# Kernel optimization log

Measured on AMD Instinct MI355X. Metric: run time of the kernel, lower is better.

## Reference

```python
import jax, jax.numpy as jnp
import numpy as np

B, S, H, L, O = 128, 2048, 128, 2, 2  # batch, seq, hidden(=input), layers, output


def setup_inputs() -> dict:
    key = jax.random.key(0)
    k1, k2, k3, k4, k5 = jax.random.split(key, 5)
    std = 1.0 / np.sqrt(H)
    x_data = jax.random.normal(k1, (B, S, H), dtype=jnp.float32)
    x_length = jax.random.randint(k2, (B,), 0, S, dtype=jnp.int32)
    x_label = jax.random.uniform(k3, (B,), dtype=jnp.float32)
    # torch Linear layout: y = x @ W.T ; init uniform(-1/sqrt(H), 1/sqrt(H))
    Wx2h = jax.random.uniform(k4, (L, 2 * H, H), minval=-std, maxval=std, dtype=jnp.float32)
    Wfc = jax.random.uniform(k5, (L, O, H), minval=-std, maxval=std, dtype=jnp.float32)
    return {"x_data": x_data, "x_length": x_length, "x_label": x_label,
            "Wx2h": Wx2h, "Wfc": Wfc}


def reference(x_data, x_length, x_label, Wx2h, Wfc):
    Bn, Sn, Hn = x_data.shape
    Ln = Wx2h.shape[0]
    # valid-timestep mask: seq index < x_length[i]
    mask = (jnp.arange(Sn)[None, :] < x_length[:, None]).astype(x_data.dtype)  # [B,S]

    def step(carry, inp):
        S1, S2 = carry            # each [L,B,H]
        x_t, m_t = inp            # [B,H], [B]
        h = x_t
        out = None
        S1_new, S2_new = [], []
        for l in range(Ln):
            gate = h @ Wx2h[l].T                    # [B,2H]
            m1, m2 = jnp.split(gate, 2, axis=1)
            s1n = S1[l] + jnp.tanh(m1)
            s2n = S2[l] + jnp.tanh(m2)
            Fu = jax.nn.relu(s1n)
            h = (1.0 - Fu) * s2n + Fu * S2[l]       # hy
            out = jax.nn.softmax(h @ Wfc[l].T, axis=1)  # [B,O]
            S1_new.append(s1n)
            S2_new.append(s2n)
        loss_t = m_t * (x_label - jax.nn.sigmoid(out[:, 1])) ** 2  # [B]
        return (jnp.stack(S1_new), jnp.stack(S2_new)), loss_t

    S0 = jnp.zeros((Ln, Bn, Hn), x_data.dtype)
    xs = (jnp.swapaxes(x_data, 0, 1), mask.T)  # time-major [S,B,H], [S,B]
    _, losses = jax.lax.scan(step, (S0, S0), xs)
    return jnp.sum(losses)
```

## Files before the change

### kernel.cpp

```cpp
#include <hip/hip_runtime.h>

typedef __bf16 bf16;
typedef __bf16 bf16x8 __attribute__((ext_vector_type(8)));
typedef float floatx4 __attribute__((ext_vector_type(4)));

#define BATCH 128
#define SEQ   2048
#define HID   128
#define TWOH  256
#define CH    128
#define NCH   16
#define MTOT  (BATCH * SEQ)

__device__ __forceinline__ float fast_tanh(float x) {
    float e = __builtin_amdgcn_exp2f(2.88539008177793f * x);
    return 1.0f - 2.0f * __builtin_amdgcn_rcpf(e + 1.0f);
}
__device__ __forceinline__ float fast_sigmoid(float x) {
    return __builtin_amdgcn_rcpf(1.0f + __builtin_amdgcn_exp2f(-1.44269504088896f * x));
}

union PK4 { unsigned long long u; bf16 h[4]; };
union PK8 { uint4 u; bf16 h[8]; };

__global__ __launch_bounds__(256) void convert_w_k(const float* __restrict__ W,
                                                   bf16* __restrict__ Wb) {
    int i = blockIdx.x * 256 + threadIdx.x;
    float4 v = ((const float4*)W)[i];
    PK4 pk;
    pk.h[0] = (bf16)v.x; pk.h[1] = (bf16)v.y;
    pk.h[2] = (bf16)v.z; pk.h[3] = (bf16)v.w;
    ((unsigned long long*)Wb)[i] = pk.u;
}

__device__ __forceinline__ void tile_prefix(const float g[4][4], float pref[4][4],
                                            float* stripe_tot, int quad, int l16) {
    float mibase = 0.f;
    #pragma unroll
    for (int mi = 0; mi < 4; ++mi) {
        float s0 = g[mi][0];
        float s1 = s0 + g[mi][1];
        float s2 = s1 + g[mi][2];
        float s3 = s2 + g[mi][3];
        float tot = s3, xq = tot;
        float t = __shfl_up(xq, 16);
        if (quad >= 1) xq += t;
        t = __shfl_up(xq, 32);
        if (quad >= 2) xq += t;
        float excl = mibase + xq - tot;
        pref[mi][0] = excl + s0;
        pref[mi][1] = excl + s1;
        pref[mi][2] = excl + s2;
        pref[mi][3] = excl + s3;
        mibase += __shfl(xq, 48 + l16);
    }
    *stripe_tot = mibase;
}


__global__ __launch_bounds__(512, 4) void l0_k(const float* __restrict__ x,
                                               const bf16* __restrict__ Wb,
                                               uint4* __restrict__ T,
                                               float* __restrict__ Pout) {
    __shared__ bf16 As[128 * 128];
    __shared__ bf16 Bs[128 * 128];
    __shared__ float psum[512];

    const int tid  = threadIdx.x;
    const int lane = tid & 63;
    const int wid  = tid >> 6;
    const int wr   = wid >> 2;
    const int wc   = wid & 3;
    const int quad = lane >> 4;
    const int l16  = lane & 15;
    const long blk = blockIdx.x;
    const long rowBase = blk * 128;

    {
        const float4* A4 = (const float4*)(x + rowBase * HID);
        #pragma unroll
        for (int it = 0; it < 8; ++it) {
            int i  = it * 512 + tid;
            int r  = i >> 5;
            int c4 = i & 31;
            float4 v = A4[i];
            int g = c4 >> 1, hf = c4 & 1;
            PK4 pk;
            pk.h[0] = (bf16)v.x; pk.h[1] = (bf16)v.y;
            pk.h[2] = (bf16)v.z; pk.h[3] = (bf16)v.w;
            *(unsigned long long*)&As[r * 128 + ((g ^ (r & 7)) << 3) + (hf << 2)] = pk.u;
        }
    }

    #pragma unroll
    for (int half = 0; half < 2; ++half) {
        __syncthreads();
        {
            const uint4* W8 = (const uint4*)(Wb + (size_t)half * 128 * HID);
            #pragma unroll
            for (int it = 0; it < 4; ++it) {
                int i = it * 512 + tid;
                int r = i >> 4;
                int g = i & 15;
                uint4 v = W8[i];
                *(uint4*)&Bs[r * 128 + ((g ^ (r & 7)) << 3)] = v;
            }
        }
        __syncthreads();

        floatx4 acc[4][2];
        #pragma unroll
        for (int a = 0; a < 4; ++a)
            #pragma unroll
            for (int b2 = 0; b2 < 2; ++b2) acc[a][b2] = (floatx4){0.f, 0.f, 0.f, 0.f};

        #pragma unroll
        for (int kk = 0; kk < 128; kk += 32) {
            bf16x8 af[4], bfr[2];
            int kg = (kk >> 3) + quad;
            #pragma unroll
            for (int mi = 0; mi < 4; ++mi) {
                int r = wr * 64 + mi * 16 + l16;
                af[mi] = *(const bf16x8*)&As[r * 128 + ((kg ^ (r & 7)) << 3)];
            }
            #pragma unroll
            for (int ni = 0; ni < 2; ++ni) {
                int n = wc * 32 + ni * 16 + l16;
                bfr[ni] = *(const bf16x8*)&Bs[n * 128 + ((kg ^ (n & 7)) << 3)];
            }
            #pragma unroll
            for (int mi = 0; mi < 4; ++mi)
                #pragma unroll
                for (int ni = 0; ni < 2; ++ni)
                    acc[mi][ni] = __builtin_amdgcn_mfma_f32_16x16x32_bf16(
                        af[mi], bfr[ni], acc[mi][ni], 0, 0, 0);
        }

        float g2[2][4][4];
        #pragma unroll
        for (int mi = 0; mi < 4; ++mi)
            #pragma unroll
            for (int ni = 0; ni < 2; ++ni)
                #pragma unroll
                for (int rr = 0; rr < 4; ++rr)
                    g2[ni][mi][rr] = fast_tanh(acc[mi][ni][rr]);

        #pragma unroll
        for (int mi = 0; mi < 4; ++mi) {
            PK8 p;
            #pragma unroll
            for (int rr = 0; rr < 4; ++rr) {
                p.h[rr]     = (bf16)g2[0][mi][rr];
                p.h[4 + rr] = (bf16)g2[1][mi][rr];
            }
            T[((blk * 2 + half) * 4 + mi) * 512 + tid] = p.u;
        }

        #pragma unroll
        for (int ni = 0; ni < 2; ++ni) {
            float cs = 0.f;
            #pragma unroll
            for (int mi = 0; mi < 4; ++mi)
                #pragma unroll
                for (int rr = 0; rr < 4; ++rr) cs += g2[ni][mi][rr];
            cs += __shfl_xor(cs, 16);
            cs += __shfl_xor(cs, 32);
            if (quad == 0)
                psum[wr * 256 + half * 128 + wc * 32 + ni * 16 + l16] = cs;
        }
    }

    __syncthreads();
    if (tid < 256) Pout[(blk << 8) + tid] = psum[tid] + psum[256 + tid];
}

__global__ __launch_bounds__(256) void scan_partials_k(float* __restrict__ P) {
    int ch = threadIdx.x;
    long b = blockIdx.x;
    float v[NCH];
    #pragma unroll
    for (int c = 0; c < NCH; ++c) v[c] = P[((b * NCH + c) << 8) + ch];
    float run = 0.f;
    #pragma unroll
    for (int c = 0; c < NCH; ++c) {
        float t = v[c];
        P[((b * NCH + c) << 8) + ch] = run;
        run += t;
    }
}

__global__ __launch_bounds__(512, 4) void l1_k(const bf16* __restrict__ Wb1,
                                               uint4* __restrict__ T,
                                               const float* __restrict__ P0,
                                               float* __restrict__ Pout) {
    __shared__ bf16 As[128 * 128];
    __shared__ bf16 Bs[128 * 128];
    __shared__ float auxp[128];
    __shared__ float psum[512];

    const int tid  = threadIdx.x;
    const int lane = tid & 63;
    const int wid  = tid >> 6;
    const int wr   = wid >> 2;
    const int wc   = wid & 3;
    const int quad = lane >> 4;
    const int l16  = lane & 15;
    const long blk = blockIdx.x;

    float p1[2][4][4];

    {
        float g2[2][4][4];
        #pragma unroll
        for (int mi = 0; mi < 4; ++mi) {
            PK8 p;
            p.u = T[((blk * 2 + 0) * 4 + mi) * 512 + tid];
            #pragma unroll
            for (int rr = 0; rr < 4; ++rr) {
                g2[0][mi][rr] = (float)p.h[rr];
                g2[1][mi][rr] = (float)p.h[4 + rr];
            }
        }
        float pref[2][4][4], st[2];
        #pragma unroll
        for (int ni = 0; ni < 2; ++ni) {
            tile_prefix(g2[ni], pref[ni], &st[ni], quad, l16);
            if (wr == 0 && quad == 0) auxp[wc * 32 + ni * 16 + l16] = st[ni];
        }
        __syncthreads();
        #pragma unroll
        for (int ni = 0; ni < 2; ++ni) {
            int col = wc * 32 + ni * 16 + l16;
            float off = P0[(blk << 8) + col];
            if (wr) off += auxp[col];
            #pragma unroll
            for (int mi = 0; mi < 4; ++mi)
                #pragma unroll
                for (int rr = 0; rr < 4; ++rr)
                    p1[ni][mi][rr] = pref[ni][mi][rr] + off;
        }
    }
    __syncthreads();

    {
        float g2[2][4][4];
        #pragma unroll
        for (int mi = 0; mi < 4; ++mi) {
            PK8 p;
            p.u = T[((blk * 2 + 1) * 4 + mi) * 512 + tid];
            #pragma unroll
            for (int rr = 0; rr < 4; ++rr) {
                g2[0][mi][rr] = (float)p.h[rr];
                g2[1][mi][rr] = (float)p.h[4 + rr];
            }
        }
        float pref[2][4][4], st[2];
        #pragma unroll
        for (int ni = 0; ni < 2; ++ni) {
            tile_prefix(g2[ni], pref[ni], &st[ni], quad, l16);
            if (wr == 0 && quad == 0) auxp[wc * 32 + ni * 16 + l16] = st[ni];
        }
        __syncthreads();
        #pragma unroll
        for (int ni = 0; ni < 2; ++ni) {
            int col = wc * 32 + ni * 16 + l16;
            int gsw = col >> 3, rem = col & 7;
            float off = P0[(blk << 8) + 128 + col];
            if (wr) off += auxp[col];
            #pragma unroll
            for (int mi = 0; mi < 4; ++mi)
                #pragma unroll
                for (int rr = 0; rr < 4; ++rr) {
                    int row = wr * 64 + mi * 16 + quad * 4 + rr;
                    float h = pref[ni][mi][rr] + off -
                              fmaxf(p1[ni][mi][rr], 0.f) * g2[ni][mi][rr];
                    As[row * 128 + ((gsw ^ (row & 7)) << 3) + rem] = (bf16)h;
                }
        }
    }

    #pragma unroll
    for (int half = 0; half < 2; ++half) {
        __syncthreads();
        {
            const uint4* W8 = (const uint4*)(Wb1 + (size_t)half * 128 * HID);
            #pragma unroll
            for (int it = 0; it < 4; ++it) {
                int i = it * 512 + tid;
                int r = i >> 4;
                int g = i & 15;
                uint4 v = W8[i];
                *(uint4*)&Bs[r * 128 + ((g ^ (r & 7)) << 3)] = v;
            }
        }
        __syncthreads();

        floatx4 acc[4][2];
        #pragma unroll
        for (int a = 0; a < 4; ++a)
            #pragma unroll
            for (int b2 = 0; b2 < 2; ++b2) acc[a][b2] = (floatx4){0.f, 0.f, 0.f, 0.f};

        #pragma unroll
        for (int kk = 0; kk < 128; kk += 32) {
            bf16x8 af[4], bfr[2];
            int kg = (kk >> 3) + quad;
            #pragma unroll
            for (int mi = 0; mi < 4; ++mi) {
                int r = wr * 64 + mi * 16 + l16;
                af[mi] = *(const bf16x8*)&As[r * 128 + ((kg ^ (r & 7)) << 3)];
            }
            #pragma unroll
            for (int ni = 0; ni < 2; ++ni) {
                int n = wc * 32 + ni * 16 + l16;
                bfr[ni] = *(const bf16x8*)&Bs[n * 128 + ((kg ^ (n & 7)) << 3)];
            }
            #pragma unroll
            for (int mi = 0; mi < 4; ++mi)
                #pragma unroll
                for (int ni = 0; ni < 2; ++ni)
                    acc[mi][ni] = __builtin_amdgcn_mfma_f32_16x16x32_bf16(
                        af[mi], bfr[ni], acc[mi][ni], 0, 0, 0);
        }

        float g2[2][4][4];
        #pragma unroll
        for (int mi = 0; mi < 4; ++mi)
            #pragma unroll
            for (int ni = 0; ni < 2; ++ni)
                #pragma unroll
                for (int rr = 0; rr < 4; ++rr)
                    g2[ni][mi][rr] = fast_tanh(acc[mi][ni][rr]);

        #pragma unroll
        for (int mi = 0; mi < 4; ++mi) {
            PK8 p;
            #pragma unroll
            for (int rr = 0; rr < 4; ++rr) {
                p.h[rr]     = (bf16)g2[0][mi][rr];
                p.h[4 + rr] = (bf16)g2[1][mi][rr];
            }
            T[((blk * 2 + half) * 4 + mi) * 512 + tid] = p.u;
        }

        #pragma unroll
        for (int ni = 0; ni < 2; ++ni) {
            float cs = 0.f;
            #pragma unroll
            for (int mi = 0; mi < 4; ++mi)
                #pragma unroll
                for (int rr = 0; rr < 4; ++rr) cs += g2[ni][mi][rr];
            cs += __shfl_xor(cs, 16);
            cs += __shfl_xor(cs, 32);
            if (quad == 0)
                psum[wr * 256 + half * 128 + wc * 32 + ni * 16 + l16] = cs;
        }
    }

    __syncthreads();
    if (tid < 256) Pout[(blk << 8) + tid] = psum[tid] + psum[256 + tid];
}

__global__ __launch_bounds__(512, 4) void loss_k(const uint4* __restrict__ T,
                                                 const float* __restrict__ P1,
                                                 const float* __restrict__ Wfc,
                                                 const int* __restrict__ xlen,
                                                 const float* __restrict__ xlab,
                                                 float* __restrict__ out) {
    __shared__ float auxp[128];
    __shared__ float zbuf[4][128][2];
    __shared__ float red[2];

    const int tid  = threadIdx.x;
    const int lane = tid & 63;
    const int wid  = tid >> 6;
    const int wr   = wid >> 2;
    const int wc   = wid & 3;
    const int quad = lane >> 4;
    const int l16  = lane & 15;
    const long blk = blockIdx.x;

    float p1[2][4][4];

    {
        float g2[2][4][4];
        #pragma unroll
        for (int mi = 0; mi < 4; ++mi) {
            PK8 p;
            p.u = T[((blk * 2 + 0) * 4 + mi) * 512 + tid];
            #pragma unroll
            for (int rr = 0; rr < 4; ++rr) {
                g2[0][mi][rr] = (float)p.h[rr];
                g2[1][mi][rr] = (float)p.h[4 + rr];
            }
        }
        float pref[2][4][4], st[2];
        #pragma unroll
        for (int ni = 0; ni < 2; ++ni) {
            tile_prefix(g2[ni], pref[ni], &st[ni], quad, l16);
            if (wr == 0 && quad == 0) auxp[wc * 32 + ni * 16 + l16] = st[ni];
        }
        __syncthreads();
        #pragma unroll
        for (int ni = 0; ni < 2; ++ni) {
            int col = wc * 32 + ni * 16 + l16;
            float off = P1[(blk << 8) + col];
            if (wr) off += auxp[col];
            #pragma unroll
            for (int mi = 0; mi < 4; ++mi)
                #pragma unroll
                for (int rr = 0; rr < 4; ++rr)
                    p1[ni][mi][rr] = pref[ni][mi][rr] + off;
        }
    }
    __syncthreads();

    {
        float g2[2][4][4];
        #pragma unroll
        for (int mi = 0; mi < 4; ++mi) {
            PK8 p;
            p.u = T[((blk * 2 + 1) * 4 + mi) * 512 + tid];
            #pragma unroll
            for (int rr = 0; rr < 4; ++rr) {
                g2[0][mi][rr] = (float)p.h[rr];
                g2[1][mi][rr] = (float)p.h[4 + rr];
            }
        }
        float pref[2][4][4], st[2];
        #pragma unroll
        for (int ni = 0; ni < 2; ++ni) {
            tile_prefix(g2[ni], pref[ni], &st[ni], quad, l16);
            if (wr == 0 && quad == 0) auxp[wc * 32 + ni * 16 + l16] = st[ni];
        }
        __syncthreads();

        float w0[2], w1[2], off[2];
        #pragma unroll
        for (int ni = 0; ni < 2; ++ni) {
            int col = wc * 32 + ni * 16 + l16;
            w0[ni] = Wfc[2 * HID + col];
            w1[ni] = Wfc[3 * HID + col];
            off[ni] = P1[(blk << 8) + 128 + col];
            if (wr) off[ni] += auxp[col];
        }
        #pragma unroll
        for (int mi = 0; mi < 4; ++mi)
            #pragma unroll
            for (int rr = 0; rr < 4; ++rr) {
                float z0 = 0.f, z1 = 0.f;
                #pragma unroll
                for (int ni = 0; ni < 2; ++ni) {
                    float h = pref[ni][mi][rr] + off[ni] -
                              fmaxf(p1[ni][mi][rr], 0.f) * g2[ni][mi][rr];
                    z0 += h * w0[ni];
                    z1 += h * w1[ni];
                }
                z0 += __shfl_xor(z0, 1); z1 += __shfl_xor(z1, 1);
                z0 += __shfl_xor(z0, 2); z1 += __shfl_xor(z1, 2);
                z0 += __shfl_xor(z0, 4); z1 += __shfl_xor(z1, 4);
                z0 += __shfl_xor(z0, 8); z1 += __shfl_xor(z1, 8);
                if (l16 == 0) {
                    int row = wr * 64 + mi * 16 + quad * 4 + rr;
                    zbuf[wc][row][0] = z0;
                    zbuf[wc][row][1] = z1;
                }
            }
    }

    __syncthreads();
    float lsum = 0.f;
    if (tid < 128) {
        int row = tid;
        int b = (int)(blk >> 4), chunk = (int)(blk & 15);
        float z0 = zbuf[0][row][0] + zbuf[1][row][0] + zbuf[2][row][0] + zbuf[3][row][0];
        float z1 = zbuf[0][row][1] + zbuf[1][row][1] + zbuf[2][row][1] + zbuf[3][row][1];
        float o1 = fast_sigmoid(z1 - z0);
        float sg = fast_sigmoid(o1);
        float d = xlab[b] - sg;
        if (chunk * CH + row < xlen[b]) lsum = d * d;
        lsum += __shfl_xor(lsum, 1);
        lsum += __shfl_xor(lsum, 2);
        lsum += __shfl_xor(lsum, 4);
        lsum += __shfl_xor(lsum, 8);
        lsum += __shfl_xor(lsum, 16);
        lsum += __shfl_xor(lsum, 32);
        if (lane == 0) red[wid] = lsum;
    }
    __syncthreads();
    if (tid == 0) atomicAdd(out, red[0] + red[1]);
}

extern "C" void kernel_launch(void* const* d_in, const int* in_sizes, int n_in,
                              void* d_out, int out_size, void* d_ws, size_t ws_size,
                              hipStream_t stream) {
    const float* x    = (const float*)d_in[0];
    const int*   xlen = (const int*)d_in[1];
    const float* xlab = (const float*)d_in[2];
    const float* Wx2h = (const float*)d_in[3];
    const float* Wfc  = (const float*)d_in[4];
    float* out = (float*)d_out;

    char* ws = (char*)d_ws;
    uint4* T  = (uint4*)ws;
    float* P0 = (float*)(ws + (size_t)MTOT * TWOH * 2);
    float* P1 = P0 + (size_t)BATCH * NCH * TWOH;
    bf16*  Wb = (bf16*)(P1 + (size_t)BATCH * NCH * TWOH);

    hipMemsetAsync(d_out, 0, sizeof(float), stream);
    convert_w_k<<<64, 256, 0, stream>>>(Wx2h, Wb);

    l0_k<<<MTOT / 128, 512, 0, stream>>>(x, Wb, T, P0);
    scan_partials_k<<<BATCH, 256, 0, stream>>>(P0);
    l1_k<<<MTOT / 128, 512, 0, stream>>>(Wb + (size_t)TWOH * HID, T, P0, P1);
    scan_partials_k<<<BATCH, 256, 0, stream>>>(P1);
    loss_k<<<MTOT / 128, 512, 0, stream>>>(T, P1, Wfc, xlen, xlab, out);
}
```

Before: 340.6 us.

## Keep weight fragments in registers and fold chunk-offset scan into consumers

The GEMM kernels now load their weight B-fragments directly from global memory into registers instead of staging them through a 32KB shared tile. This removes two barriers per half and halves LDS use, which may allow more resident blocks. The separate scan_partials kernels are also removed: each l1/loss block sums the preceding chunk partials itself into shared memory. That saves two launches, at the cost of redundant global reads that grow to as many as 15 per column.

```diff
diff --git a/kernel.cpp b/kernel.cpp
--- a/kernel.cpp
+++ b/kernel.cpp
@@ -57,13 +57,44 @@
     *stripe_tot = mibase;
 }
 
+__device__ __forceinline__ void load_wf(const bf16* __restrict__ Wh, bf16x8 wf[4][2],
+                                        int wc, int quad, int l16) {
+    #pragma unroll
+    for (int s = 0; s < 4; ++s)
+        #pragma unroll
+        for (int ni = 0; ni < 2; ++ni) {
+            int n = wc * 32 + ni * 16 + l16;
+            int kg = s * 4 + quad;
+            wf[s][ni] = *(const bf16x8*)&Wh[n * 128 + kg * 8];
+        }
+}
+
+__device__ __forceinline__ void gemm_tile(const bf16* As, const bf16x8 wf[4][2],
+                                          floatx4 acc[4][2], int wr, int quad, int l16) {
+    #pragma unroll
+    for (int s = 0; s < 4; ++s) {
+        int kg = s * 4 + quad;
+        bf16x8 af[4];
+        #pragma unroll
+        for (int mi = 0; mi < 4; ++mi) {
+            int r = wr * 64 + mi * 16 + l16;
+            af[mi] = *(const bf16x8*)&As[r * 128 + ((kg ^ (r & 7)) << 3)];
+        }
+        #pragma unroll
+        for (int mi = 0; mi < 4; ++mi)
+            #pragma unroll
+            for (int ni = 0; ni < 2; ++ni)
+                acc[mi][ni] = __builtin_amdgcn_mfma_f32_16x16x32_bf16(
+                    af[mi], wf[s][ni], acc[mi][ni], 0, 0, 0);
+    }
+}
+
 
 __global__ __launch_bounds__(512, 4) void l0_k(const float* __restrict__ x,
                                                const bf16* __restrict__ Wb,
                                                uint4* __restrict__ T,
                                                float* __restrict__ Pout) {
     __shared__ bf16 As[128 * 128];
-    __shared__ bf16 Bs[128 * 128];
     __shared__ float psum[512];
 
     const int tid  = threadIdx.x;
@@ -92,49 +123,21 @@
         }
     }
 
+    bf16x8 wf[4][2];
+    load_wf(Wb, wf, wc, quad, l16);
+    __syncthreads();
+
     #pragma unroll
     for (int half = 0; half < 2; ++half) {
-        __syncthreads();
-        {
-            const uint4* W8 = (const uint4*)(Wb + (size_t)half * 128 * HID);
-            #pragma unroll
-            for (int it = 0; it < 4; ++it) {
-                int i = it * 512 + tid;
-                int r = i >> 4;
-                int g = i & 15;
-                uint4 v = W8[i];
-                *(uint4*)&Bs[r * 128 + ((g ^ (r & 7)) << 3)] = v;
-            }
-        }
-        __syncthreads();
-
         floatx4 acc[4][2];
         #pragma unroll
         for (int a = 0; a < 4; ++a)
             #pragma unroll
             for (int b2 = 0; b2 < 2; ++b2) acc[a][b2] = (floatx4){0.f, 0.f, 0.f, 0.f};
 
-        #pragma unroll
-        for (int kk = 0; kk < 128; kk += 32) {
-            bf16x8 af[4], bfr[2];
-            int kg = (kk >> 3) + quad;
-            #pragma unroll
-            for (int mi = 0; mi < 4; ++mi) {
-                int r = wr * 64 + mi * 16 + l16;
-                af[mi] = *(const bf16x8*)&As[r * 128 + ((kg ^ (r & 7)) << 3)];
-            }
-            #pragma unroll
-            for (int ni = 0; ni < 2; ++ni) {
-                int n = wc * 32 + ni * 16 + l16;
-                bfr[ni] = *(const bf16x8*)&Bs[n * 128 + ((kg ^ (n & 7)) << 3)];
-            }
-            #pragma unroll
-            for (int mi = 0; mi < 4; ++mi)
-                #pragma unroll
-                for (int ni = 0; ni < 2; ++ni)
-                    acc[mi][ni] = __builtin_amdgcn_mfma_f32_16x16x32_bf16(
-                        af[mi], bfr[ni], acc[mi][ni], 0, 0, 0);
-        }
+        gemm_tile(As, wf, acc, wr, quad, l16);
+        if (half == 0)
+            load_wf(Wb + (size_t)128 * HID, wf, wc, quad, l16);
 
         float g2[2][4][4];
         #pragma unroll
@@ -174,27 +177,12 @@
     if (tid < 256) Pout[(blk << 8) + tid] = psum[tid] + psum[256 + tid];
 }
 
-__global__ __launch_bounds__(256) void scan_partials_k(float* __restrict__ P) {
-    int ch = threadIdx.x;
-    long b = blockIdx.x;
-    float v[NCH];
-    #pragma unroll
-    for (int c = 0; c < NCH; ++c) v[c] = P[((b * NCH + c) << 8) + ch];
-    float run = 0.f;
-    #pragma unroll
-    for (int c = 0; c < NCH; ++c) {
-        float t = v[c];
-        P[((b * NCH + c) << 8) + ch] = run;
-        run += t;
-    }
-}
-
 __global__ __launch_bounds__(512, 4) void l1_k(const bf16* __restrict__ Wb1,
                                                uint4* __restrict__ T,
                                                const float* __restrict__ P0,
                                                float* __restrict__ Pout) {
     __shared__ bf16 As[128 * 128];
-    __shared__ bf16 Bs[128 * 128];
+    __shared__ float offP[256];
     __shared__ float auxp[128];
     __shared__ float psum[512];
 
@@ -206,6 +194,15 @@
     const int quad = lane >> 4;
     const int l16  = lane & 15;
     const long blk = blockIdx.x;
+    const int  bb  = (int)(blk >> 4);
+    const int  cc  = (int)(blk & 15);
+
+    if (tid < 256) {
+        float a = 0.f;
+        for (int cp = 0; cp < cc; ++cp)
+            a += P0[(((long)(bb * NCH + cp)) << 8) + tid];
+        offP[tid] = a;
+    }
 
     float p1[2][4][4];
 
@@ -231,7 +228,7 @@
         #pragma unroll
         for (int ni = 0; ni < 2; ++ni) {
             int col = wc * 32 + ni * 16 + l16;
-            float off = P0[(blk << 8) + col];
+            float off = offP[col];
             if (wr) off += auxp[col];
             #pragma unroll
             for (int mi = 0; mi < 4; ++mi)
@@ -265,7 +262,7 @@
         for (int ni = 0; ni < 2; ++ni) {
             int col = wc * 32 + ni * 16 + l16;
             int gsw = col >> 3, rem = col & 7;
-            float off = P0[(blk << 8) + 128 + col];
+            float off = offP[128 + col];
             if (wr) off += auxp[col];
             #pragma unroll
             for (int mi = 0; mi < 4; ++mi)
@@ -279,49 +276,21 @@
         }
     }
 
+    bf16x8 wf[4][2];
+    load_wf(Wb1, wf, wc, quad, l16);
+    __syncthreads();
+
     #pragma unroll
     for (int half = 0; half < 2; ++half) {
-        __syncthreads();
-        {
-            const uint4* W8 = (const uint4*)(Wb1 + (size_t)half * 128 * HID);
-            #pragma unroll
-            for (int it = 0; it < 4; ++it) {
-                int i = it * 512 + tid;
-                int r = i >> 4;
-                int g = i & 15;
-                uint4 v = W8[i];
-                *(uint4*)&Bs[r * 128 + ((g ^ (r & 7)) << 3)] = v;
-            }
-        }
-        __syncthreads();
-
         floatx4 acc[4][2];
         #pragma unroll
         for (int a = 0; a < 4; ++a)
             #pragma unroll
             for (int b2 = 0; b2 < 2; ++b2) acc[a][b2] = (floatx4){0.f, 0.f, 0.f, 0.f};
 
-        #pragma unroll
-        for (int kk = 0; kk < 128; kk += 32) {
-            bf16x8 af[4], bfr[2];
-            int kg = (kk >> 3) + quad;
-            #pragma unroll
-            for (int mi = 0; mi < 4; ++mi) {
-                int r = wr * 64 + mi * 16 + l16;
-                af[mi] = *(const bf16x8*)&As[r * 128 + ((kg ^ (r & 7)) << 3)];
-            }
-            #pragma unroll
-            for (int ni = 0; ni < 2; ++ni) {
-                int n = wc * 32 + ni * 16 + l16;
-                bfr[ni] = *(const bf16x8*)&Bs[n * 128 + ((kg ^ (n & 7)) << 3)];
-            }
-            #pragma unroll
-            for (int mi = 0; mi < 4; ++mi)
-                #pragma unroll
-                for (int ni = 0; ni < 2; ++ni)
-                    acc[mi][ni] = __builtin_amdgcn_mfma_f32_16x16x32_bf16(
-                        af[mi], bfr[ni], acc[mi][ni], 0, 0, 0);
-        }
+        gemm_tile(As, wf, acc, wr, quad, l16);
+        if (half == 0)
+            load_wf(Wb1 + (size_t)128 * HID, wf, wc, quad, l16);
 
         float g2[2][4][4];
         #pragma unroll
@@ -367,6 +336,7 @@
                                                  const int* __restrict__ xlen,
                                                  const float* __restrict__ xlab,
                                                  float* __restrict__ out) {
+    __shared__ float offP[256];
     __shared__ float auxp[128];
     __shared__ float zbuf[4][128][2];
     __shared__ float red[2];
@@ -379,6 +349,15 @@
     const int quad = lane >> 4;
     const int l16  = lane & 15;
     const long blk = blockIdx.x;
+    const int  bb  = (int)(blk >> 4);
+    const int  cc  = (int)(blk & 15);
+
+    if (tid < 256) {
+        float a = 0.f;
+        for (int cp = 0; cp < cc; ++cp)
+            a += P1[(((long)(bb * NCH + cp)) << 8) + tid];
+        offP[tid] = a;
+    }
 
     float p1[2][4][4];
 
@@ -404,7 +383,7 @@
         #pragma unroll
         for (int ni = 0; ni < 2; ++ni) {
             int col = wc * 32 + ni * 16 + l16;
-            float off = P1[(blk << 8) + col];
+            float off = offP[col];
             if (wr) off += auxp[col];
             #pragma unroll
             for (int mi = 0; mi < 4; ++mi)
@@ -441,7 +420,7 @@
             int col = wc * 32 + ni * 16 + l16;
             w0[ni] = Wfc[2 * HID + col];
             w1[ni] = Wfc[3 * HID + col];
-            off[ni] = P1[(blk << 8) + 128 + col];
+            off[ni] = offP[128 + col];
             if (wr) off[ni] += auxp[col];
         }
         #pragma unroll
@@ -472,13 +451,12 @@
     float lsum = 0.f;
     if (tid < 128) {
         int row = tid;
-        int b = (int)(blk >> 4), chunk = (int)(blk & 15);
         float z0 = zbuf[0][row][0] + zbuf[1][row][0] + zbuf[2][row][0] + zbuf[3][row][0];
         float z1 = zbuf[0][row][1] + zbuf[1][row][1] + zbuf[2][row][1] + zbuf[3][row][1];
         float o1 = fast_sigmoid(z1 - z0);
         float sg = fast_sigmoid(o1);
-        float d = xlab[b] - sg;
-        if (chunk * CH + row < xlen[b]) lsum = d * d;
+        float d = xlab[bb] - sg;
+        if (cc * CH + row < xlen[bb]) lsum = d * d;
         lsum += __shfl_xor(lsum, 1);
         lsum += __shfl_xor(lsum, 2);
         lsum += __shfl_xor(lsum, 4);
@@ -511,8 +489,6 @@
     convert_w_k<<<64, 256, 0, stream>>>(Wx2h, Wb);
 
     l0_k<<<MTOT / 128, 512, 0, stream>>>(x, Wb, T, P0);
-    scan_partials_k<<<BATCH, 256, 0, stream>>>(P0);
     l1_k<<<MTOT / 128, 512, 0, stream>>>(Wb + (size_t)TWOH * HID, T, P0, P1);
-    scan_partials_k<<<BATCH, 256, 0, stream>>>(P1);
     loss_k<<<MTOT / 128, 512, 0, stream>>>(T, P1, Wfc, xlen, xlab, out);
 }
```

Measured after the change: 366.3 us. 1.08x slower.
